# Optimization experiments

Measured on AMD Instinct MI355X. Metric: run time of the kernel, lower is better.

The kernel has to match this reference:

```python
import jax, jax.numpy as jnp
import numpy as np

DIM = 768
HEADS = 12
HEAD_DIM = DIM // HEADS
SCALE = HEAD_DIM ** -0.5


def setup_inputs() -> dict:
    key = jax.random.key(0)
    k1, k2, k3, k4, k5 = jax.random.split(key, 5)
    x = jax.random.normal(k1, (8, 1024, DIM), dtype=jnp.float32)
    # torch Linear default init ~ U(-1/sqrt(fan_in), 1/sqrt(fan_in)); scale similarly
    s = 1.0 / np.sqrt(DIM)
    qkv_w = jax.random.uniform(k2, (3 * DIM, DIM), minval=-s, maxval=s, dtype=jnp.float32)
    qkv_b = jax.random.uniform(k3, (3 * DIM,), minval=-s, maxval=s, dtype=jnp.float32)
    proj_w = jax.random.uniform(k4, (DIM, DIM), minval=-s, maxval=s, dtype=jnp.float32)
    proj_b = jax.random.uniform(k5, (DIM,), minval=-s, maxval=s, dtype=jnp.float32)
    return {"x": x, "qkv_w": qkv_w, "qkv_b": qkv_b, "proj_w": proj_w, "proj_b": proj_b}


def reference(x, qkv_w, qkv_b, proj_w, proj_b):
    B, N, C = x.shape
    qkv = x @ qkv_w.T + qkv_b                      # [B, N, 3C]
    qkv = qkv.reshape(B, N, 3, HEADS, HEAD_DIM)
    q = jnp.transpose(qkv[:, :, 0], (0, 2, 1, 3))  # [B, H, N, D]
    k = jnp.transpose(qkv[:, :, 1], (0, 2, 1, 3))
    v = jnp.transpose(qkv[:, :, 2], (0, 2, 1, 3))
    attn = jnp.einsum('bhnd,bhmd->bhnm', q, k) * SCALE  # [B, H, N, N]
    attn = jax.nn.softmax(attn, axis=-1)
    out = jnp.einsum('bhnm,bhmd->bhnd', attn, v)   # [B, H, N, D]
    out = jnp.transpose(out, (0, 2, 1, 3)).reshape(B, N, C)
    return out @ proj_w.T + proj_b
```

## Files before the change

kernel.cpp:

```cpp
#include <hip/hip_runtime.h>
#include <stdint.h>

typedef unsigned short ushort_t;
typedef __attribute__((ext_vector_type(8))) short short8;
typedef __attribute__((ext_vector_type(4))) float f32x4;
typedef __attribute__((address_space(1))) uint32_t as1_u32;
typedef __attribute__((address_space(3))) uint32_t as3_u32;

#define MFMA16(a, b, c) __builtin_amdgcn_mfma_f32_16x16x32_bf16(a, b, c, 0, 0, 0)

#define PIPE_BAR4() asm volatile("s_waitcnt vmcnt(4)\n\ts_barrier" ::: "memory")
#define PIPE_BAR6() asm volatile("s_waitcnt vmcnt(6)\n\ts_barrier" ::: "memory")
#define PIPE_BAR0() asm volatile("s_waitcnt vmcnt(0)\n\ts_barrier" ::: "memory")
#define BAR_RAW()   asm volatile("s_barrier" ::: "memory")

__device__ __forceinline__ void cp16(const void* g, void* l) {
    __builtin_amdgcn_global_load_lds((as1_u32*)(uintptr_t)g,
                                     (as3_u32*)(uint32_t)(uintptr_t)l, 16, 0, 0);
}

__device__ __forceinline__ ushort_t f2bf(float f) {
    uint32_t u = __float_as_uint(f);
    u += 0x7fffu + ((u >> 16) & 1u);
    return (ushort_t)(u >> 16);
}

__global__ __launch_bounds__(256) void cvt3_kernel(const float* __restrict__ x,
                                                   const float* __restrict__ w1,
                                                   const float* __restrict__ w2,
                                                   ushort_t* __restrict__ xb,
                                                   ushort_t* __restrict__ wb1,
                                                   ushort_t* __restrict__ wb2) {
    const int bid = blockIdx.x;
    const float4* src;
    ushort4* dst;
    int i;
    if (bid < 6144)      { src = (const float4*)x;  dst = (ushort4*)xb;  i = bid * 256 + threadIdx.x; }
    else if (bid < 7872) { src = (const float4*)w1; dst = (ushort4*)wb1; i = (bid - 6144) * 256 + threadIdx.x; }
    else                 { src = (const float4*)w2; dst = (ushort4*)wb2; i = (bid - 7872) * 256 + threadIdx.x; }
    float4 v = src[i];
    ushort4 o;
    o.x = f2bf(v.x); o.y = f2bf(v.y); o.z = f2bf(v.z); o.w = f2bf(v.w);
    dst[i] = o;
}

__global__ __launch_bounds__(256) void qkv_gemm(const ushort_t* __restrict__ xb,
                                                const ushort_t* __restrict__ wq,
                                                const float* __restrict__ bias,
                                                ushort_t* __restrict__ Qg,
                                                ushort_t* __restrict__ Kg,
                                                ushort_t* __restrict__ Vt) {
    __shared__ __align__(16) ushort_t smem[17408];
    const int t = threadIdx.x, w = t >> 6, lane = t & 63;
    const int m16 = lane & 15, q = lane >> 4;
    const int n0 = blockIdx.x * 128, m0 = blockIdx.y * 128;
    const int wm = w >> 1, wn = w & 1;
    ushort_t* const A0 = smem;
    ushort_t* const B0 = smem + 4096;
    ushort_t* const A1 = smem + 8192;
    ushort_t* const B1 = smem + 12288;

    f32x4 acc[4][4];
#pragma unroll
    for (int i = 0; i < 4; ++i)
#pragma unroll
        for (int j = 0; j < 4; ++j) acc[i][j] = (f32x4)0.f;

    auto issueT = [&](int kk, ushort_t* As, ushort_t* Bs) {
#pragma unroll
        for (int s = 0; s < 2; ++s) {
            const int i2 = s * 256 + t;
            const int lb = (s * 256 + w * 64) * 8;
            cp16(&xb[(m0 + (i2 >> 2)) * 768 + kk + (i2 & 3) * 8], &As[lb]);
            cp16(&wq[(n0 + (i2 >> 2)) * 768 + kk + (i2 & 3) * 8], &Bs[lb]);
        }
    };

    issueT(0, A0, B0);
    issueT(32, A1, B1);
#pragma unroll 2
    for (int kki = 0; kki < 24; ++kki) {
        if (kki < 23) { PIPE_BAR4(); } else { PIPE_BAR0(); }
        ushort_t* As = (kki & 1) ? A1 : A0;
        ushort_t* Bs = (kki & 1) ? B1 : B0;
        short8 a[4], b[4];
#pragma unroll
        for (int i = 0; i < 4; ++i) a[i] = *(const short8*)&As[(wm * 64 + i * 16 + m16) * 32 + q * 8];
#pragma unroll
        for (int j = 0; j < 4; ++j) b[j] = *(const short8*)&Bs[(wn * 64 + j * 16 + m16) * 32 + q * 8];
#pragma unroll
        for (int i = 0; i < 4; ++i)
#pragma unroll
            for (int j = 0; j < 4; ++j) acc[i][j] = MFMA16(a[i], b[j], acc[i][j]);
        BAR_RAW();
        if (kki < 22) issueT((kki + 2) * 32, As, Bs);
    }

    const int three = n0 / 768;
    const int b_idx = m0 >> 10;

    if (three < 2) {
        ushort_t* dst = three ? Kg : Qg;
        const float scale = three ? 1.0f : 0.18033688011112042f;
#pragma unroll
        for (int j = 0; j < 4; ++j) {
            float bj = bias[n0 + wn * 64 + j * 16 + m16];
#pragma unroll
            for (int i = 0; i < 4; ++i)
#pragma unroll
                for (int r = 0; r < 4; ++r)
                    smem[(wm * 64 + i * 16 + q * 4 + r) * 136 + wn * 64 + j * 16 + m16] =
                        f2bf((acc[i][j][r] + bj) * scale);
        }
        __syncthreads();
        const int col0 = n0 - three * 768;
#pragma unroll
        for (int u8 = 0; u8 < 8; ++u8) {
            int u = u8 * 256 + t;
            int row = u >> 4, cg = u & 15;
            uint4 vv = *(const uint4*)&smem[row * 136 + cg * 8];
            int col = col0 + cg * 8;
            int hh = col >> 6, dd = col & 63;
            int n = (m0 & 1023) + row;
            *(uint4*)&dst[((b_idx * 12 + hh) * 1024 + n) * 64 + dd] = vv;
        }
    } else {
        const int nq_base = (m0 & 1023) + wm * 64;
#pragma unroll
        for (int j = 0; j < 4; ++j) {
            int col = n0 + wn * 64 + j * 16 + m16 - 1536;
            float bj = bias[col + 1536];
            int hh = col >> 6, dd = col & 63;
            ushort_t* base = Vt + ((b_idx * 12 + hh) * 64 + dd) * 1024;
#pragma unroll
            for (int i = 0; i < 4; ++i) {
                ushort4 pk;
                pk.x = f2bf(acc[i][j][0] + bj);
                pk.y = f2bf(acc[i][j][1] + bj);
                pk.z = f2bf(acc[i][j][2] + bj);
                pk.w = f2bf(acc[i][j][3] + bj);
                *(ushort4*)&base[nq_base + i * 16 + q * 4] = pk;
            }
        }
    }
}

__global__ __launch_bounds__(256) void attn_kernel(const ushort_t* __restrict__ Qg,
                                                   const ushort_t* __restrict__ Kg,
                                                   const ushort_t* __restrict__ Vt,
                                                   ushort_t* __restrict__ Og) {
    __shared__ __align__(16) ushort_t Ks[128 * 64];
    __shared__ __align__(16) ushort_t Vs[64 * 128];
    __shared__ __align__(16) ushort_t Ps[4 * 16 * 136];
    const int t = threadIdx.x, w = t >> 6, lane = t & 63;
    const int m16 = lane & 15, q = lane >> 4;
    const int qt = blockIdx.x, bh = blockIdx.y;
    const int b = bh / 12, h = bh % 12;
    const ushort_t* Qbh = Qg + bh * 65536;
    const ushort_t* Kbh = Kg + bh * 65536;
    const ushort_t* Vbh = Vt + bh * 65536;
    ushort_t* Pw = &Ps[w * 2176];

    const int q0 = qt * 128 + w * 32;
    short8 qf[2][2];
#pragma unroll
    for (int i = 0; i < 2; ++i)
#pragma unroll
        for (int kd = 0; kd < 2; ++kd)
            qf[i][kd] = *(const short8*)&Qbh[(q0 + i * 16 + m16) * 64 + kd * 32 + q * 8];

    f32x4 o[2][4];
#pragma unroll
    for (int i = 0; i < 2; ++i)
#pragma unroll
        for (int ds = 0; ds < 4; ++ds) o[i][ds] = (f32x4)0.f;
    float l_run[2] = {0.f, 0.f};

    for (int kt = 0; kt < 8; ++kt) {
        const int key0 = kt * 128;
#pragma unroll
        for (int p = 0; p < 4; ++p) {
            const int c = p * 256 + t;
            const int lbase = (p * 256 + w * 64) * 8;
            { int key = c >> 3, g = c & 7;
              cp16(&Kbh[(key0 + key) * 64 + ((g ^ (key & 7)) * 8)], &Ks[lbase]); }
            { int d = c >> 4, g2 = c & 15;
              cp16(&Vbh[d * 1024 + key0 + ((g2 ^ (d & 15)) * 8)], &Vs[lbase]); }
        }
        __syncthreads();

        f32x4 st[2][8];
#pragma unroll
        for (int ks = 0; ks < 8; ++ks) {
            const ushort_t* kr = &Ks[(ks * 16 + m16) * 64];
            short8 a0 = *(const short8*)&kr[(q ^ (m16 & 7)) * 8];
            short8 a1 = *(const short8*)&kr[((4 + q) ^ (m16 & 7)) * 8];
            st[0][ks] = MFMA16(a1, qf[0][1], MFMA16(a0, qf[0][0], (f32x4)0.f));
            st[1][ks] = MFMA16(a1, qf[1][1], MFMA16(a0, qf[1][0], (f32x4)0.f));
        }

#pragma unroll
        for (int i = 0; i < 2; ++i) {
            float ps = 0.f;
#pragma unroll
            for (int ks = 0; ks < 8; ++ks) {
                float p0 = exp2f(st[i][ks][0]);
                float p1 = exp2f(st[i][ks][1]);
                float p2 = exp2f(st[i][ks][2]);
                float p3 = exp2f(st[i][ks][3]);
                ps += (p0 + p1) + (p2 + p3);
                uint32_t u0 = __float_as_uint(p0) + 0x8000u;
                uint32_t u1 = __float_as_uint(p1) + 0x8000u;
                uint32_t u2 = __float_as_uint(p2) + 0x8000u;
                uint32_t u3 = __float_as_uint(p3) + 0x8000u;
                uint2 pk;
                pk.x = __builtin_amdgcn_perm(u1, u0, 0x07060302u);
                pk.y = __builtin_amdgcn_perm(u3, u2, 0x07060302u);
                *(uint2*)&Pw[m16 * 136 + ks * 16 + q * 4] = pk;
            }
            ps += __shfl_xor(ps, 16, 64);
            ps += __shfl_xor(ps, 32, 64);
            l_run[i] += ps;
#pragma unroll
            for (int kkk = 0; kkk < 4; ++kkk) {
                short8 ap = *(const short8*)&Pw[m16 * 136 + kkk * 32 + q * 8];
#pragma unroll
                for (int ds = 0; ds < 4; ++ds) {
                    short8 vb = *(const short8*)&Vs[(ds * 16 + m16) * 128 + (((kkk * 4 + q) ^ m16) * 8)];
                    o[i][ds] = MFMA16(ap, vb, o[i][ds]);
                }
            }
        }
        __syncthreads();
    }
#pragma unroll
    for (int i = 0; i < 2; ++i) {
        float linv = 1.f / l_run[i];
#pragma unroll
        for (int r = 0; r < 4; ++r) {
            float lr = __shfl(linv, q * 4 + r, 64);
            int row = b * 1024 + q0 + i * 16 + q * 4 + r;
#pragma unroll
            for (int ds = 0; ds < 4; ++ds)
                Og[row * 768 + h * 64 + ds * 16 + m16] = f2bf(o[i][ds][r] * lr);
        }
    }
}

__global__ __launch_bounds__(128) void proj_gemm(const ushort_t* __restrict__ Ob,
                                                 const ushort_t* __restrict__ wp,
                                                 const float* __restrict__ bias,
                                                 float* __restrict__ out) {
    __shared__ __align__(16) ushort_t smem[12288];
    const int t = threadIdx.x, w = t >> 6, lane = t & 63;
    const int m16 = lane & 15, q = lane >> 4;
    const int n0 = blockIdx.x * 64, m0 = blockIdx.y * 128;
    ushort_t* const A0 = smem;
    ushort_t* const B0 = smem + 4096;
    ushort_t* const A1 = smem + 6144;
    ushort_t* const B1 = smem + 10240;

    f32x4 acc[4][4];
#pragma unroll
    for (int i = 0; i < 4; ++i)
#pragma unroll
        for (int j = 0; j < 4; ++j) acc[i][j] = (f32x4)0.f;

    auto issueT = [&](int kk, ushort_t* As, ushort_t* Bs) {
#pragma unroll
        for (int s = 0; s < 4; ++s) {
            const int c = s * 128 + t;
            cp16(&Ob[(m0 + (c >> 2)) * 768 + kk + (c & 3) * 8], &As[(s * 128 + w * 64) * 8]);
        }
#pragma unroll
        for (int s = 0; s < 2; ++s) {
            const int c = s * 128 + t;
            cp16(&wp[(n0 + (c >> 2)) * 768 + kk + (c & 3) * 8], &Bs[(s * 128 + w * 64) * 8]);
        }
    };

    issueT(0, A0, B0);
    issueT(32, A1, B1);
#pragma unroll 2
    for (int kki = 0; kki < 24; ++kki) {
        if (kki < 23) { PIPE_BAR6(); } else { PIPE_BAR0(); }
        ushort_t* As = (kki & 1) ? A1 : A0;
        ushort_t* Bs = (kki & 1) ? B1 : B0;
        short8 a[4], b[4];
#pragma unroll
        for (int i = 0; i < 4; ++i) a[i] = *(const short8*)&As[(w * 64 + i * 16 + m16) * 32 + q * 8];
#pragma unroll
        for (int j = 0; j < 4; ++j) b[j] = *(const short8*)&Bs[(j * 16 + m16) * 32 + q * 8];
#pragma unroll
        for (int i = 0; i < 4; ++i)
#pragma unroll
            for (int j = 0; j < 4; ++j) acc[i][j] = MFMA16(a[i], b[j], acc[i][j]);
        BAR_RAW();
        if (kki < 22) issueT((kki + 2) * 32, As, Bs);
    }

#pragma unroll
    for (int j = 0; j < 4; ++j) {
        int col = n0 + j * 16 + m16;
        float bj = bias[col];
#pragma unroll
        for (int i = 0; i < 4; ++i)
#pragma unroll
            for (int r = 0; r < 4; ++r) {
                int row = m0 + w * 64 + i * 16 + q * 4 + r;
                out[row * 768 + col] = acc[i][j][r] + bj;
            }
    }
}

extern "C" void kernel_launch(void* const* d_in, const int* in_sizes, int n_in,
                              void* d_out, int out_size, void* d_ws, size_t ws_size,
                              hipStream_t stream) {
    const float* x      = (const float*)d_in[0];
    const float* qkv_w  = (const float*)d_in[1];
    const float* qkv_b  = (const float*)d_in[2];
    const float* proj_w = (const float*)d_in[3];
    const float* proj_b = (const float*)d_in[4];
    float* out = (float*)d_out;

    char* ws = (char*)d_ws;
    ushort_t* xb    = (ushort_t*)(ws);
    ushort_t* wqkv  = (ushort_t*)(ws + 12582912);
    ushort_t* wproj = (ushort_t*)(ws + 16121856);
    ushort_t* Qg    = (ushort_t*)(ws + 17301504);
    ushort_t* Kg    = (ushort_t*)(ws + 29884416);
    ushort_t* Vt    = (ushort_t*)(ws + 42467328);
    ushort_t* Og    = (ushort_t*)(ws + 55050240);

    cvt3_kernel<<<8448, 256, 0, stream>>>(x, qkv_w, proj_w, xb, wqkv, wproj);
    qkv_gemm<<<dim3(18, 64), 256, 0, stream>>>(xb, wqkv, qkv_b, Qg, Kg, Vt);
    attn_kernel<<<dim3(8, 96), 256, 0, stream>>>(Qg, Kg, Vt, Og);
    proj_gemm<<<dim3(12, 64), 128, 0, stream>>>(Og, wproj, proj_b, out);
}
```

Before: 211.2 us.

## Prefetch next K/V tiles in attention to overlap loads with compute

The attention kernel's K/V tile loads move out of the head of each iteration. The next K tile is now issued right after the QK^T MFMAs, and the next V tile right after the PV MFMAs. Fine-grained vmcnt waits with barriers replace the two full __syncthreads, so global-to-LDS transfers overlap with softmax and matmul work. It keeps single LDS buffers, so correctness depends on the barrier placement and the order of the vmcnt counts.

```diff
diff --git a/kernel.cpp b/kernel.cpp
--- a/kernel.cpp
+++ b/kernel.cpp
@@ -9,10 +9,11 @@
 
 #define MFMA16(a, b, c) __builtin_amdgcn_mfma_f32_16x16x32_bf16(a, b, c, 0, 0, 0)
 
+#define PIPE_BAR6() asm volatile("s_waitcnt vmcnt(6)\n\ts_barrier" ::: "memory")
 #define PIPE_BAR4() asm volatile("s_waitcnt vmcnt(4)\n\ts_barrier" ::: "memory")
-#define PIPE_BAR6() asm volatile("s_waitcnt vmcnt(6)\n\ts_barrier" ::: "memory")
 #define PIPE_BAR0() asm volatile("s_waitcnt vmcnt(0)\n\ts_barrier" ::: "memory")
 #define BAR_RAW()   asm volatile("s_barrier" ::: "memory")
+#define BAR_LGKM()  asm volatile("s_waitcnt lgkmcnt(0)\n\ts_barrier" ::: "memory")
 
 __device__ __forceinline__ void cp16(const void* g, void* l) {
     __builtin_amdgcn_global_load_lds((as1_u32*)(uintptr_t)g,
@@ -169,6 +170,23 @@
         for (int kd = 0; kd < 2; ++kd)
             qf[i][kd] = *(const short8*)&Qbh[(q0 + i * 16 + m16) * 64 + kd * 32 + q * 8];
 
+    auto issueK = [&](int key0) {
+#pragma unroll
+        for (int p = 0; p < 4; ++p) {
+            const int c = p * 256 + t;
+            const int key = c >> 3, g = c & 7;
+            cp16(&Kbh[(key0 + key) * 64 + ((g ^ (key & 7)) * 8)], &Ks[(p * 256 + w * 64) * 8]);
+        }
+    };
+    auto issueV = [&](int key0) {
+#pragma unroll
+        for (int p = 0; p < 4; ++p) {
+            const int c = p * 256 + t;
+            const int d = c >> 4, g2 = c & 15;
+            cp16(&Vbh[d * 1024 + key0 + ((g2 ^ (d & 15)) * 8)], &Vs[(p * 256 + w * 64) * 8]);
+        }
+    };
+
     f32x4 o[2][4];
 #pragma unroll
     for (int i = 0; i < 2; ++i)
@@ -176,18 +194,10 @@
         for (int ds = 0; ds < 4; ++ds) o[i][ds] = (f32x4)0.f;
     float l_run[2] = {0.f, 0.f};
 
+    issueK(0);
+    issueV(0);
     for (int kt = 0; kt < 8; ++kt) {
-        const int key0 = kt * 128;
-#pragma unroll
-        for (int p = 0; p < 4; ++p) {
-            const int c = p * 256 + t;
-            const int lbase = (p * 256 + w * 64) * 8;
-            { int key = c >> 3, g = c & 7;
-              cp16(&Kbh[(key0 + key) * 64 + ((g ^ (key & 7)) * 8)], &Ks[lbase]); }
-            { int d = c >> 4, g2 = c & 15;
-              cp16(&Vbh[d * 1024 + key0 + ((g2 ^ (d & 15)) * 8)], &Vs[lbase]); }
-        }
-        __syncthreads();
+        if (kt) { PIPE_BAR4(); } else { PIPE_BAR0(); }
 
         f32x4 st[2][8];
 #pragma unroll
@@ -198,9 +208,10 @@
             st[0][ks] = MFMA16(a1, qf[0][1], MFMA16(a0, qf[0][0], (f32x4)0.f));
             st[1][ks] = MFMA16(a1, qf[1][1], MFMA16(a0, qf[1][0], (f32x4)0.f));
         }
-
-#pragma unroll
-        for (int i = 0; i < 2; ++i) {
+        BAR_LGKM();
+        if (kt < 7) issueK((kt + 1) * 128);
+
+        auto softmax_pack = [&](int i) {
             float ps = 0.f;
 #pragma unroll
             for (int ks = 0; ks < 8; ++ks) {
@@ -221,6 +232,8 @@
             ps += __shfl_xor(ps, 16, 64);
             ps += __shfl_xor(ps, 32, 64);
             l_run[i] += ps;
+        };
+        auto pv = [&](int i) {
 #pragma unroll
             for (int kkk = 0; kkk < 4; ++kkk) {
                 short8 ap = *(const short8*)&Pw[m16 * 136 + kkk * 32 + q * 8];
@@ -230,8 +243,15 @@
                     o[i][ds] = MFMA16(ap, vb, o[i][ds]);
                 }
             }
-        }
-        __syncthreads();
+        };
+
+        softmax_pack(0);
+        if (kt < 7) { PIPE_BAR4(); } else { PIPE_BAR0(); }
+        pv(0);
+        softmax_pack(1);
+        pv(1);
+        BAR_LGKM();
+        if (kt < 7) issueV((kt + 1) * 128);
     }
 #pragma unroll
     for (int i = 0; i < 2; ++i) {
```

Result: no change. 212.6 us (+0.7%).

## Keep softmax probabilities in registers and feed PV with 16x16x16 MFMA

Applied to the files above, without the earlier changes.

The attention kernel stops writing the exponentiated scores to a per-wave LDS buffer and reading them back as MFMA operands. The packed bf16 probabilities from each 16x16 S tile are fed directly as the A operand of the 16x16x16 bf16 MFMA, whose input layout matches the output layout of the 16x16x32 QK MFMA. V is read from LDS in 8-byte chunks instead. The QK MFMAs are also moved inside the per-row-block loop, so each wave recomputes S per row block while reusing its K fragment loads. This removes the LDS round trip and frees shared memory, but it doubles the number of PV MFMA instructions because each one has half the K depth, and it issues more V LDS reads.

```diff
diff --git a/kernel.cpp b/kernel.cpp
--- a/kernel.cpp
+++ b/kernel.cpp
@@ -3,14 +3,17 @@
 
 typedef unsigned short ushort_t;
 typedef __attribute__((ext_vector_type(8))) short short8;
+typedef __attribute__((ext_vector_type(4))) short short4v;
 typedef __attribute__((ext_vector_type(4))) float f32x4;
+typedef __attribute__((ext_vector_type(2))) uint32_t u32x2;
 typedef __attribute__((address_space(1))) uint32_t as1_u32;
 typedef __attribute__((address_space(3))) uint32_t as3_u32;
 
-#define MFMA16(a, b, c) __builtin_amdgcn_mfma_f32_16x16x32_bf16(a, b, c, 0, 0, 0)
-
+#define MFMA16(a, b, c)  __builtin_amdgcn_mfma_f32_16x16x32_bf16(a, b, c, 0, 0, 0)
+#define MFMA1K(a, b, c)  __builtin_amdgcn_mfma_f32_16x16x16bf16_1k(a, b, c, 0, 0, 0)
+
+#define PIPE_BAR6() asm volatile("s_waitcnt vmcnt(6)\n\ts_barrier" ::: "memory")
 #define PIPE_BAR4() asm volatile("s_waitcnt vmcnt(4)\n\ts_barrier" ::: "memory")
-#define PIPE_BAR6() asm volatile("s_waitcnt vmcnt(6)\n\ts_barrier" ::: "memory")
 #define PIPE_BAR0() asm volatile("s_waitcnt vmcnt(0)\n\ts_barrier" ::: "memory")
 #define BAR_RAW()   asm volatile("s_barrier" ::: "memory")
 
@@ -151,7 +154,6 @@
                                                    ushort_t* __restrict__ Og) {
     __shared__ __align__(16) ushort_t Ks[128 * 64];
     __shared__ __align__(16) ushort_t Vs[64 * 128];
-    __shared__ __align__(16) ushort_t Ps[4 * 16 * 136];
     const int t = threadIdx.x, w = t >> 6, lane = t & 63;
     const int m16 = lane & 15, q = lane >> 4;
     const int qt = blockIdx.x, bh = blockIdx.y;
@@ -159,7 +161,6 @@
     const ushort_t* Qbh = Qg + bh * 65536;
     const ushort_t* Kbh = Kg + bh * 65536;
     const ushort_t* Vbh = Vt + bh * 65536;
-    ushort_t* Pw = &Ps[w * 2176];
 
     const int q0 = qt * 128 + w * 32;
     short8 qf[2][2];
@@ -181,53 +182,49 @@
 #pragma unroll
         for (int p = 0; p < 4; ++p) {
             const int c = p * 256 + t;
-            const int lbase = (p * 256 + w * 64) * 8;
             { int key = c >> 3, g = c & 7;
-              cp16(&Kbh[(key0 + key) * 64 + ((g ^ (key & 7)) * 8)], &Ks[lbase]); }
+              cp16(&Kbh[(key0 + key) * 64 + ((g ^ (key & 7)) * 8)], &Ks[c * 8]); }
             { int d = c >> 4, g2 = c & 15;
-              cp16(&Vbh[d * 1024 + key0 + ((g2 ^ (d & 15)) * 8)], &Vs[lbase]); }
+              cp16(&Vbh[d * 1024 + key0 + ((g2 ^ (d & 15)) * 8)], &Vs[c * 8]); }
         }
         __syncthreads();
 
-        f32x4 st[2][8];
-#pragma unroll
-        for (int ks = 0; ks < 8; ++ks) {
-            const ushort_t* kr = &Ks[(ks * 16 + m16) * 64];
-            short8 a0 = *(const short8*)&kr[(q ^ (m16 & 7)) * 8];
-            short8 a1 = *(const short8*)&kr[((4 + q) ^ (m16 & 7)) * 8];
-            st[0][ks] = MFMA16(a1, qf[0][1], MFMA16(a0, qf[0][0], (f32x4)0.f));
-            st[1][ks] = MFMA16(a1, qf[1][1], MFMA16(a0, qf[1][0], (f32x4)0.f));
-        }
-
 #pragma unroll
         for (int i = 0; i < 2; ++i) {
+            u32x2 pk[8];
             float ps = 0.f;
 #pragma unroll
             for (int ks = 0; ks < 8; ++ks) {
-                float p0 = exp2f(st[i][ks][0]);
-                float p1 = exp2f(st[i][ks][1]);
-                float p2 = exp2f(st[i][ks][2]);
-                float p3 = exp2f(st[i][ks][3]);
+                const ushort_t* kr = &Ks[(ks * 16 + m16) * 64];
+                short8 a0 = *(const short8*)&kr[(q ^ (m16 & 7)) * 8];
+                short8 a1 = *(const short8*)&kr[((4 + q) ^ (m16 & 7)) * 8];
+                f32x4 c = MFMA16(a1, qf[i][1], MFMA16(a0, qf[i][0], (f32x4)0.f));
+                float p0 = exp2f(c[0]);
+                float p1 = exp2f(c[1]);
+                float p2 = exp2f(c[2]);
+                float p3 = exp2f(c[3]);
                 ps += (p0 + p1) + (p2 + p3);
                 uint32_t u0 = __float_as_uint(p0) + 0x8000u;
                 uint32_t u1 = __float_as_uint(p1) + 0x8000u;
                 uint32_t u2 = __float_as_uint(p2) + 0x8000u;
                 uint32_t u3 = __float_as_uint(p3) + 0x8000u;
-                uint2 pk;
-                pk.x = __builtin_amdgcn_perm(u1, u0, 0x07060302u);
-                pk.y = __builtin_amdgcn_perm(u3, u2, 0x07060302u);
-                *(uint2*)&Pw[m16 * 136 + ks * 16 + q * 4] = pk;
+                u32x2 pp;
+                pp.x = __builtin_amdgcn_perm(u1, u0, 0x07060302u);
+                pp.y = __builtin_amdgcn_perm(u3, u2, 0x07060302u);
+                pk[ks] = pp;
             }
             ps += __shfl_xor(ps, 16, 64);
             ps += __shfl_xor(ps, 32, 64);
             l_run[i] += ps;
-#pragma unroll
-            for (int kkk = 0; kkk < 4; ++kkk) {
-                short8 ap = *(const short8*)&Pw[m16 * 136 + kkk * 32 + q * 8];
+
+#pragma unroll
+            for (int ks = 0; ks < 8; ++ks) {
+                const int vidx = m16 * 128 + (((2 * ks + (q >> 1)) ^ m16) * 8) + 4 * (q & 1);
+                short4v ap = __builtin_bit_cast(short4v, pk[ks]);
 #pragma unroll
                 for (int ds = 0; ds < 4; ++ds) {
-                    short8 vb = *(const short8*)&Vs[(ds * 16 + m16) * 128 + (((kkk * 4 + q) ^ m16) * 8)];
-                    o[i][ds] = MFMA16(ap, vb, o[i][ds]);
+                    short4v vb = *(const short4v*)&Vs[ds * 2048 + vidx];
+                    o[i][ds] = MFMA1K(ap, vb, o[i][ds]);
                 }
             }
         }
```

Result: slower. 216.1 us (+2.3%).
